# Optimization experiments

Hardware: AMD Instinct MI355X
Metric: run time of the kernel (lower is better)

## Reference

```python
import jax, jax.numpy as jnp
import numpy as np

B, N, C = 32, 577, 768
H = 12
DH = C // H  # 64
SCALE = DH ** -0.5


def setup_inputs() -> dict:
    key = jax.random.key(0)
    ks = jax.random.split(key, 5)
    x = jax.random.normal(ks[0], (B, N, C), dtype=jnp.float32)
    # Linear params (torch convention: y = x @ W.T + b)
    qkv_w = jax.random.normal(ks[1], (3 * C, C), dtype=jnp.float32) * (C ** -0.5)
    qkv_b = jnp.zeros((3 * C,), dtype=jnp.float32)
    proj_w = jax.random.normal(ks[2], (C, C), dtype=jnp.float32) * (C ** -0.5)
    proj_b = jnp.zeros((C,), dtype=jnp.float32)
    return {"x": x, "qkv_w": qkv_w, "qkv_b": qkv_b, "proj_w": proj_w, "proj_b": proj_b}


def reference(x, qkv_w, qkv_b, proj_w, proj_b):
    b, n, c = x.shape
    qkv = x @ qkv_w.T + qkv_b                       # [B, N, 3C]
    qkv = qkv.reshape(b, n, 3, H, DH).transpose(2, 0, 3, 1, 4)  # [3, B, H, N, DH]
    q, k, v = qkv[0], qkv[1], qkv[2]
    q = q * SCALE
    attn = jnp.einsum('bhnd,bhmd->bhnm', q, k)      # [B, H, N, N]
    # sigmoid -> inverse-sigmoid straight-through rewrite (forward equals logit(sigmoid(attn)))
    sig = jax.nn.sigmoid(attn)
    inv_sig = jnp.log(sig / (1.0 - sig))
    attn_st = attn + jax.lax.stop_gradient(inv_sig - attn)
    p = jax.nn.softmax(attn_st, axis=-1)
    out = jnp.einsum('bhnm,bhmd->bhnd', p, v)       # [B, H, N, DH]
    out = out.transpose(0, 2, 1, 3).reshape(b, n, c)
    return out @ proj_w.T + proj_b
```

## Files before the change

### kernel.cpp

```cpp
#include <hip/hip_runtime.h>

typedef __bf16 bf16;
typedef __attribute__((ext_vector_type(4))) __bf16 bf16x4;
typedef __attribute__((ext_vector_type(8))) __bf16 bf16x8;
typedef __attribute__((ext_vector_type(4))) float f32x4;

#define MFMA_BF16(A_, B_, C_) __builtin_amdgcn_mfma_f32_16x16x32_bf16(A_, B_, C_, 0, 0, 0)

#define BB    32
#define SEQ   577
#define CH    768
#define NH    12
#define DHD   64
#define MROWS (BB * SEQ)
#define NQKV  2304
#define SEQP  584
#define QSCALE 0.1803368801111204f

#define NT (CH / 64)

__device__ __forceinline__ void async_ld16(const bf16* g, bf16* l) {
  __builtin_amdgcn_global_load_lds(
      (const __attribute__((address_space(1))) void*)g,
      (__attribute__((address_space(3))) void*)l, 16, 0, 0);
}

__global__ __launch_bounds__(256) void cvt_bf16(const float* __restrict__ src,
                                                bf16* __restrict__ dst, int n) {
  int idx = (blockIdx.x * 256 + threadIdx.x) * 4;
  if (idx >= n) return;
  float4 v = *(const float4*)(src + idx);
  bf16x4 o = {(bf16)v.x, (bf16)v.y, (bf16)v.z, (bf16)v.w};
  *(bf16x4*)(dst + idx) = o;
}

template <int EPI>
__global__ __launch_bounds__(512, 2)
void gemm_bt(const bf16* __restrict__ A, const bf16* __restrict__ W,
             const float* __restrict__ bias,
             bf16* __restrict__ qrm, bf16* __restrict__ krm, bf16* __restrict__ vt,
             float* __restrict__ out) {
  __shared__ bf16 As[2][2][256 * 32];
  __shared__ bf16 Bs[2][2][256 * 32];
  const int tid = threadIdx.x, lane = tid & 63, wid = tid >> 6;
  const int quad = lane >> 4, r15 = lane & 15;

  const int nbx = (int)gridDim.x;
  const int nwg = nbx * (int)gridDim.y;
  int bid = (int)blockIdx.y * nbx + (int)blockIdx.x;
  int q8 = nwg >> 3, r8 = nwg & 7;
  int xcd = bid & 7, sub = bid >> 3;
  int wg = (xcd < r8 ? xcd * (q8 + 1) : r8 * (q8 + 1) + (xcd - r8) * q8) + sub;
  const int m0 = (wg / nbx) * 256, n0 = (wg % nbx) * 256;

  const int rm = (wid >> 2) * 128;
  const int rn = (wid & 3) * 64;

  int aOff[4], bOff[4];
#pragma unroll
  for (int i = 0; i < 4; ++i) {
    int slot = i * 512 + tid;
    int row = (slot >> 2) & 255, ks = slot >> 10, pc2 = slot & 3;
    int gc2 = pc2 ^ ((row ^ (row >> 2)) & 3);
    aOff[i] = (m0 + row) * CH + ks * 32 + gc2 * 8;
    bOff[i] = (n0 + row) * CH + ks * 32 + gc2 * 8;
  }

  f32x4 acc[8][4];
#pragma unroll
  for (int i = 0; i < 8; ++i)
#pragma unroll
    for (int j = 0; j < 4; ++j) acc[i][j] = (f32x4){0.f, 0.f, 0.f, 0.f};

#define GSTAGE(K0, BUF)                                                        \
  {                                                                            \
    _Pragma("unroll") for (int i = 0; i < 4; ++i) {                            \
      async_ld16(A + aOff[i] + (K0), &As[BUF][0][(i * 512 + tid) * 8]);        \
      async_ld16(W + bOff[i] + (K0), &Bs[BUF][0][(i * 512 + tid) * 8]);        \
    }                                                                          \
  }

#define GCOMPUTE(BUF)                                                          \
  {                                                                            \
    bf16x8 bfr[4][2];                                                          \
    _Pragma("unroll") for (int sn = 0; sn < 4; ++sn) {                         \
      int fr = rn + sn * 16 + r15;                                             \
      int pc2 = quad ^ ((fr ^ (fr >> 2)) & 3);                                 \
      bfr[sn][0] = *(const bf16x8*)(&Bs[BUF][0][fr * 32 + pc2 * 8]);           \
      bfr[sn][1] = *(const bf16x8*)(&Bs[BUF][1][fr * 32 + pc2 * 8]);           \
    }                                                                          \
    _Pragma("unroll") for (int sp = 0; sp < 4; ++sp) {                         \
      bf16x8 af[2][2];                                                         \
      _Pragma("unroll") for (int s2 = 0; s2 < 2; ++s2) {                       \
        int fr = rm + (sp * 2 + s2) * 16 + r15;                                \
        int pc2 = quad ^ ((fr ^ (fr >> 2)) & 3);                               \
        af[s2][0] = *(const bf16x8*)(&As[BUF][0][fr * 32 + pc2 * 8]);          \
        af[s2][1] = *(const bf16x8*)(&As[BUF][1][fr * 32 + pc2 * 8]);          \
      }                                                                        \
      _Pragma("unroll") for (int s2 = 0; s2 < 2; ++s2)                         \
        _Pragma("unroll") for (int sn = 0; sn < 4; ++sn) {                     \
          acc[sp * 2 + s2][sn] =                                               \
              MFMA_BF16(af[s2][0], bfr[sn][0], acc[sp * 2 + s2][sn]);          \
          acc[sp * 2 + s2][sn] =                                               \
              MFMA_BF16(af[s2][1], bfr[sn][1], acc[sp * 2 + s2][sn]);          \
        }                                                                      \
    }                                                                          \
  }

  GSTAGE(0, 0);
  for (int t = 0; t < NT; ++t) {
    int buf = t & 1;
    __syncthreads();
    if (t + 1 < NT) GSTAGE((t + 1) * 64, buf ^ 1);
    GCOMPUTE(buf);
  }

  if (EPI == 0) {
    int tcl = (n0 >= 1536) ? 2 : (n0 >= 768 ? 1 : 0);
#pragma unroll
    for (int sn = 0; sn < 4; ++sn) {
      int gn = n0 + rn + sn * 16 + r15;
      float bv = bias[gn];
      int col = gn - tcl * CH;
      int h = col >> 6, d = col & 63;
#pragma unroll
      for (int sm = 0; sm < 8; ++sm) {
        int gmBase = m0 + rm + sm * 16 + quad * 4;
#pragma unroll
        for (int r = 0; r < 4; ++r) {
          int gm = gmBase + r;
          if (gm < MROWS) {
            float v = acc[sm][sn][r] + bv;
            if (tcl == 0) {
              qrm[(size_t)gm * CH + col] = (bf16)(v * QSCALE);
            } else if (tcl == 1) {
              krm[(size_t)gm * CH + col] = (bf16)v;
            } else {
              int b_ = gm / SEQ;
              int n_ = gm - b_ * SEQ;
              vt[((size_t)(b_ * NH + h) * DHD + d) * SEQP + n_] = (bf16)v;
            }
          }
        }
      }
    }
  } else {
#pragma unroll
    for (int sn = 0; sn < 4; ++sn) {
      int gn = n0 + rn + sn * 16 + r15;
      float bv = bias[gn];
#pragma unroll
      for (int sm = 0; sm < 8; ++sm) {
        int gmBase = m0 + rm + sm * 16 + quad * 4;
#pragma unroll
        for (int r = 0; r < 4; ++r) {
          int gm = gmBase + r;
          if (gm < MROWS) out[(size_t)gm * CH + gn] = acc[sm][sn][r] + bv;
        }
      }
    }
  }
}

__global__ __launch_bounds__(256, 6)
void attn_kernel(const bf16* __restrict__ qrm, const bf16* __restrict__ krm,
                 const bf16* __restrict__ vt, bf16* __restrict__ ob) {
  __shared__ bf16 Ks[64 * 72];
  __shared__ bf16 Vt[64 * 72];
  const int tid = threadIdx.x, lane = tid & 63, wid = tid >> 6;
  const int quad = lane >> 4, r15 = lane & 15;
  const int qt = blockIdx.x, bh = blockIdx.y;
  const int b_ = bh / NH, h = bh - b_ * NH;
  const bf16* vtb = vt + (size_t)bh * DHD * SEQP;

  int qrow = qt * 64 + wid * 16 + r15;
  if (qrow > SEQ - 1) qrow = SEQ - 1;
  const bf16* qp = qrm + (size_t)(b_ * SEQ + qrow) * CH + h * DHD + quad * 8;
  bf16x8 qf0 = *(const bf16x8*)qp;
  bf16x8 qf1 = *(const bf16x8*)(qp + 32);

  f32x4 oacc[4];
#pragma unroll
  for (int i = 0; i < 4; ++i) oacc[i] = (f32x4){0.f, 0.f, 0.f, 0.f};
  float lrow[4] = {0.f, 0.f, 0.f, 0.f};

  for (int j0 = 0; j0 < SEQ; j0 += 64) {
    __syncthreads();
#pragma unroll
    for (int c = 0; c < 2; ++c) {
      int sid = c * 256 + tid;
      int row = sid >> 3, cc = sid & 7;
      int jr = j0 + row;
      if (jr > SEQ - 1) jr = SEQ - 1;
      *(bf16x8*)(Ks + row * 72 + cc * 8) =
          *(const bf16x8*)(krm + (size_t)(b_ * SEQ + jr) * CH + h * DHD + cc * 8);
      int jst = j0 + cc * 8;
      if (jst > SEQ - 1) jst = SEQ - 1;
      *(bf16x8*)(Vt + row * 72 + cc * 8) = *(const bf16x8*)(vtb + (size_t)row * SEQP + jst);
    }
    __syncthreads();

    f32x4 s[4];
#pragma unroll
    for (int sj = 0; sj < 4; ++sj) {
      bf16x8 kf0 = *(const bf16x8*)(Ks + (sj * 16 + r15) * 72 + quad * 8);
      bf16x8 kf1 = *(const bf16x8*)(Ks + (sj * 16 + r15) * 72 + 32 + quad * 8);
      f32x4 z = (f32x4){0.f, 0.f, 0.f, 0.f};
      s[sj] = MFMA_BF16(qf0, kf0, z);
      s[sj] = MFMA_BF16(qf1, kf1, s[sj]);
    }
#pragma unroll
    for (int sj = 0; sj < 4; ++sj)
      if (j0 + sj * 16 + r15 > SEQ - 1) s[sj] = (f32x4){-1e30f, -1e30f, -1e30f, -1e30f};

#pragma unroll
    for (int sj = 0; sj < 4; ++sj)
#pragma unroll
      for (int r = 0; r < 4; ++r) {
        float e = __builtin_amdgcn_exp2f(s[sj][r]);
        s[sj][r] = e;
        lrow[r] += e;
      }

    __syncthreads();
    bf16* Pw = Ks + wid * (16 * 72);
#pragma unroll
    for (int sj = 0; sj < 4; ++sj)
#pragma unroll
      for (int r = 0; r < 4; ++r)
        Pw[(quad * 4 + r) * 72 + sj * 16 + r15] = (bf16)s[sj][r];
    asm volatile("s_waitcnt lgkmcnt(0)" ::: "memory");

#pragma unroll
    for (int kc = 0; kc < 2; ++kc) {
      bf16x8 pf = *(const bf16x8*)(Pw + r15 * 72 + kc * 32 + quad * 8);
#pragma unroll
      for (int sd = 0; sd < 4; ++sd) {
        bf16x8 vf = *(const bf16x8*)(Vt + (sd * 16 + r15) * 72 + kc * 32 + quad * 8);
        oacc[sd] = MFMA_BF16(pf, vf, oacc[sd]);
      }
    }
  }

#pragma unroll
  for (int r = 0; r < 4; ++r) {
    float rs = lrow[r];
    rs += __shfl_xor(rs, 1);
    rs += __shfl_xor(rs, 2);
    rs += __shfl_xor(rs, 4);
    rs += __shfl_xor(rs, 8);
    lrow[r] = rs;
  }

#pragma unroll
  for (int r = 0; r < 4; ++r) {
    int orow = qt * 64 + wid * 16 + quad * 4 + r;
    if (orow < SEQ) {
      float inv = 1.0f / lrow[r];
      size_t rowoff = ((size_t)(b_ * SEQ + orow)) * CH + h * DHD;
#pragma unroll
      for (int sd = 0; sd < 4; ++sd)
        ob[rowoff + sd * 16 + r15] = (bf16)(oacc[sd][r] * inv);
    }
  }
}

extern "C" void kernel_launch(void* const* d_in, const int* in_sizes, int n_in,
                              void* d_out, int out_size, void* d_ws, size_t ws_size,
                              hipStream_t stream) {
  const float* x      = (const float*)d_in[0];
  const float* qkv_w  = (const float*)d_in[1];
  const float* qkv_b  = (const float*)d_in[2];
  const float* proj_w = (const float*)d_in[3];
  const float* proj_b = (const float*)d_in[4];
  float* out = (float*)d_out;

  char* w = (char*)d_ws;
  bf16* xb  = (bf16*)(w);
  bf16* wqp = (bf16*)(w + 28360704);
  bf16* qrm = (bf16*)(w + 31899648);
  bf16* krm = (bf16*)(w + 60260352);
  bf16* vtb = (bf16*)(w + 88621056);

  cvt_bf16<<<(MROWS * CH / 4 + 255) / 256, 256, 0, stream>>>(x, xb, MROWS * CH);
  cvt_bf16<<<(NQKV * CH / 4 + 255) / 256, 256, 0, stream>>>(qkv_w, wqp, NQKV * CH);

  gemm_bt<0><<<dim3(NQKV / 256, 73), 512, 0, stream>>>(
      xb, wqp, qkv_b, qrm, krm, vtb, nullptr);

  attn_kernel<<<dim3(10, BB * NH), 256, 0, stream>>>(qrm, krm, vtb, xb);

  cvt_bf16<<<(CH * CH / 4 + 255) / 256, 256, 0, stream>>>(proj_w, wqp, CH * CH);

  gemm_bt<1><<<dim3(CH / 256, 73), 512, 0, stream>>>(
      xb, wqp, proj_b, nullptr, nullptr, nullptr, out);
}
```

Before: 415.9 us.

## Replace double-buffered GEMM K-loop with 4-slot ring and prefetch depth two

The templated bf16 GEMM used by both the QKV and output projections now steps through K in 32-wide slices instead of 64-wide ones. It uses a 4-buffer LDS ring and keeps two stages of async global-to-LDS loads in flight. Each step waits with an explicit s_waitcnt vmcnt count and a single raw s_barrier instead of __syncthreads, so memory latency overlaps MFMA work more deeply. LDS footprint is unchanged, but there are twice as many barriers per tile. The hand-tuned vmcnt counts depend on the exact number of loads issued per stage.

```diff
diff --git a/kernel.cpp b/kernel.cpp
--- a/kernel.cpp
+++ b/kernel.cpp
@@ -17,7 +17,7 @@
 #define SEQP  584
 #define QSCALE 0.1803368801111204f
 
-#define NT (CH / 64)
+#define NSTEP 24
 
 __device__ __forceinline__ void async_ld16(const bf16* g, bf16* l) {
   __builtin_amdgcn_global_load_lds(
@@ -40,8 +40,8 @@
              const float* __restrict__ bias,
              bf16* __restrict__ qrm, bf16* __restrict__ krm, bf16* __restrict__ vt,
              float* __restrict__ out) {
-  __shared__ bf16 As[2][2][256 * 32];
-  __shared__ bf16 Bs[2][2][256 * 32];
+  __shared__ bf16 As[4][256 * 32];
+  __shared__ bf16 Bs[4][256 * 32];
   const int tid = threadIdx.x, lane = tid & 63, wid = tid >> 6;
   const int quad = lane >> 4, r15 = lane & 15;
 
@@ -56,14 +56,14 @@
   const int rm = (wid >> 2) * 128;
   const int rn = (wid & 3) * 64;
 
-  int aOff[4], bOff[4];
-#pragma unroll
-  for (int i = 0; i < 4; ++i) {
+  int aOff[2], bOff[2];
+#pragma unroll
+  for (int i = 0; i < 2; ++i) {
     int slot = i * 512 + tid;
-    int row = (slot >> 2) & 255, ks = slot >> 10, pc2 = slot & 3;
+    int row = slot >> 2, pc2 = slot & 3;
     int gc2 = pc2 ^ ((row ^ (row >> 2)) & 3);
-    aOff[i] = (m0 + row) * CH + ks * 32 + gc2 * 8;
-    bOff[i] = (n0 + row) * CH + ks * 32 + gc2 * 8;
+    aOff[i] = (m0 + row) * CH + gc2 * 8;
+    bOff[i] = (n0 + row) * CH + gc2 * 8;
   }
 
   f32x4 acc[8][4];
@@ -72,47 +72,48 @@
 #pragma unroll
     for (int j = 0; j < 4; ++j) acc[i][j] = (f32x4){0.f, 0.f, 0.f, 0.f};
 
-#define GSTAGE(K0, BUF)                                                        \
+#define ISSUE(S)                                                               \
   {                                                                            \
-    _Pragma("unroll") for (int i = 0; i < 4; ++i) {                            \
-      async_ld16(A + aOff[i] + (K0), &As[BUF][0][(i * 512 + tid) * 8]);        \
-      async_ld16(W + bOff[i] + (K0), &Bs[BUF][0][(i * 512 + tid) * 8]);        \
+    const int kb_ = (S) * 32;                                                  \
+    const int bf_ = (S) & 3;                                                   \
+    _Pragma("unroll") for (int i = 0; i < 2; ++i) {                            \
+      async_ld16(A + aOff[i] + kb_, &As[bf_][(i * 512 + tid) * 8]);            \
+      async_ld16(W + bOff[i] + kb_, &Bs[bf_][(i * 512 + tid) * 8]);            \
     }                                                                          \
   }
 
-#define GCOMPUTE(BUF)                                                          \
+#define COMPUTE(BF)                                                            \
   {                                                                            \
-    bf16x8 bfr[4][2];                                                          \
+    bf16x8 bfr[4], afr[8];                                                     \
     _Pragma("unroll") for (int sn = 0; sn < 4; ++sn) {                         \
       int fr = rn + sn * 16 + r15;                                             \
       int pc2 = quad ^ ((fr ^ (fr >> 2)) & 3);                                 \
-      bfr[sn][0] = *(const bf16x8*)(&Bs[BUF][0][fr * 32 + pc2 * 8]);           \
-      bfr[sn][1] = *(const bf16x8*)(&Bs[BUF][1][fr * 32 + pc2 * 8]);           \
+      bfr[sn] = *(const bf16x8*)(&Bs[BF][fr * 32 + pc2 * 8]);                  \
     }                                                                          \
-    _Pragma("unroll") for (int sp = 0; sp < 4; ++sp) {                         \
-      bf16x8 af[2][2];                                                         \
-      _Pragma("unroll") for (int s2 = 0; s2 < 2; ++s2) {                       \
-        int fr = rm + (sp * 2 + s2) * 16 + r15;                                \
-        int pc2 = quad ^ ((fr ^ (fr >> 2)) & 3);                               \
-        af[s2][0] = *(const bf16x8*)(&As[BUF][0][fr * 32 + pc2 * 8]);          \
-        af[s2][1] = *(const bf16x8*)(&As[BUF][1][fr * 32 + pc2 * 8]);          \
-      }                                                                        \
-      _Pragma("unroll") for (int s2 = 0; s2 < 2; ++s2)                         \
-        _Pragma("unroll") for (int sn = 0; sn < 4; ++sn) {                     \
-          acc[sp * 2 + s2][sn] =                                               \
-              MFMA_BF16(af[s2][0], bfr[sn][0], acc[sp * 2 + s2][sn]);          \
-          acc[sp * 2 + s2][sn] =                                               \
-              MFMA_BF16(af[s2][1], bfr[sn][1], acc[sp * 2 + s2][sn]);          \
-        }                                                                      \
+    _Pragma("unroll") for (int sm = 0; sm < 8; ++sm) {                         \
+      int fr = rm + sm * 16 + r15;                                             \
+      int pc2 = quad ^ ((fr ^ (fr >> 2)) & 3);                                 \
+      afr[sm] = *(const bf16x8*)(&As[BF][fr * 32 + pc2 * 8]);                  \
     }                                                                          \
-  }
-
-  GSTAGE(0, 0);
-  for (int t = 0; t < NT; ++t) {
-    int buf = t & 1;
-    __syncthreads();
-    if (t + 1 < NT) GSTAGE((t + 1) * 64, buf ^ 1);
-    GCOMPUTE(buf);
+    _Pragma("unroll") for (int sm = 0; sm < 8; ++sm)                           \
+      _Pragma("unroll") for (int sn = 0; sn < 4; ++sn)                         \
+        acc[sm][sn] = MFMA_BF16(afr[sm], bfr[sn], acc[sm][sn]);                \
+  }
+
+  ISSUE(0);
+  ISSUE(1);
+  for (int s = 0; s < NSTEP; ++s) {
+    if (s < NSTEP - 2) {
+      ISSUE(s + 2);
+      asm volatile("s_waitcnt vmcnt(8)" ::: "memory");
+    } else if (s == NSTEP - 2) {
+      asm volatile("s_waitcnt vmcnt(4)" ::: "memory");
+    } else {
+      asm volatile("s_waitcnt vmcnt(0)" ::: "memory");
+    }
+    __builtin_amdgcn_s_barrier();
+    asm volatile("" ::: "memory");
+    COMPUTE(s & 3);
   }
 
   if (EPI == 0) {
```

Result: faster. 392.7 us (-5.6%).
